# Kernel tuning notes

Hardware: AMD Instinct MI355X
Metric: run time of the kernel (lower is better)

## Reference

```python
import jax, jax.numpy as jnp
import numpy as np

FP8_MAX = 448.0  # finfo(float8_e4m3fn).max

def setup_inputs() -> dict:
    key = jax.random.key(0)
    k_x, k_w, k_b = jax.random.split(key, 3)
    B, S, D_IN, D_OUT = 4, 2048, 4096, 16384
    x = jax.random.normal(k_x, (B, S, D_IN), dtype=jnp.float32)
    # Build an fp8-quantized weight exactly as FP8WeightOnlyLinear.from_linear does:
    w = jax.random.normal(k_w, (D_OUT, D_IN), dtype=jnp.float32) * 0.02
    amax = jnp.max(jnp.abs(w))
    scale = jnp.where(amax > 0, amax / FP8_MAX, 1.0)
    # round-trip through float8_e4m3fn so stored values are true fp8 codes
    w_fp8 = jnp.clip(w / scale, -FP8_MAX, FP8_MAX).astype(jnp.float8_e4m3fn)
    weight_fp8 = w_fp8.astype(jnp.float32)  # fp8-representable values, held in fp32
    weight_scale = scale.reshape(1).astype(jnp.float32)
    bias = jax.random.normal(k_b, (D_OUT,), dtype=jnp.float32) * 0.01
    return {"x": x, "weight_fp8": weight_fp8, "weight_scale": weight_scale, "bias": bias}

def reference(x, weight_fp8, weight_scale, bias):
    # w = weight_fp8.to(x.dtype) * weight_scale ; out = x @ w.T + bias
    w = weight_fp8.astype(x.dtype) * weight_scale.astype(x.dtype)  # [D_OUT, D_IN]
    out = jnp.einsum('bsd,od->bso', x, w) + bias.astype(x.dtype)
    return out
```

## Files before the change

### kernel.cpp

```cpp
#include <hip/hip_runtime.h>
#include <stdint.h>

typedef unsigned int u32;
using i32x4 = __attribute__((ext_vector_type(4))) int;

#define GLD_LDS16(SRC, DST)                                      \
  __builtin_amdgcn_global_load_lds(                              \
      (const __attribute__((address_space(1))) void*)(SRC),      \
      (__attribute__((address_space(3))) void*)(DST), 16, 0, 0)

#define SCHED0() __builtin_amdgcn_sched_barrier(0)
#define BAR()    __builtin_amdgcn_s_barrier()
#define PRIO(x)  __builtin_amdgcn_s_setprio(x)

__global__ __launch_bounds__(256)
void quant_rows(const float* __restrict__ x, const float* __restrict__ w,
                signed char* __restrict__ xq, signed char* __restrict__ wq,
                float* __restrict__ sx, float* __restrict__ sw,
                int Mrows, int totRows, int K) {
  __shared__ float red[4];
  for (int row = blockIdx.x; row < totRows; row += gridDim.x) {
    const bool isx = row < Mrows;
    const float* src = isx ? x + (size_t)row * K : w + (size_t)(row - Mrows) * K;
    const float4* s4 = reinterpret_cast<const float4*>(src) + threadIdx.x * 4;
    float4 v[4];
#pragma unroll
    for (int g = 0; g < 4; ++g) v[g] = s4[g];
    float am = 0.f;
#pragma unroll
    for (int g = 0; g < 4; ++g)
      am = fmaxf(am, fmaxf(fmaxf(fabsf(v[g].x), fabsf(v[g].y)),
                           fmaxf(fabsf(v[g].z), fabsf(v[g].w))));
#pragma unroll
    for (int m = 1; m <= 32; m <<= 1) am = fmaxf(am, __shfl_xor(am, m));
    if ((threadIdx.x & 63) == 0) red[threadIdx.x >> 6] = am;
    __syncthreads();
    am = fmaxf(fmaxf(red[0], red[1]), fmaxf(red[2], red[3]));
    const float s   = am > 0.f ? am * (1.f / 127.f) : 1.f;
    const float inv = am > 0.f ? 127.f / am : 0.f;
    u32 pk[4];
#pragma unroll
    for (int g = 0; g < 4; ++g) {
      const float* vp = reinterpret_cast<const float*>(&v[g]);
      u32 p = 0;
#pragma unroll
      for (int e = 0; e < 4; ++e) {
        int q = (int)rintf(vp[e] * inv);
        q = q < -127 ? -127 : (q > 127 ? 127 : q);
        p |= ((u32)(q & 0xff)) << (8 * e);
      }
      pk[g] = p;
    }
    signed char* dst = (isx ? xq + (size_t)row * K : wq + (size_t)(row - Mrows) * K)
                       + threadIdx.x * 16;
    *reinterpret_cast<uint4*>(dst) = make_uint4(pk[0], pk[1], pk[2], pk[3]);
    if (threadIdx.x == 0) { if (isx) sx[row] = s; else sw[row - Mrows] = s; }
    __syncthreads();
  }
}

__global__ __launch_bounds__(512, 2)
void gemm_i8_gate(const signed char* __restrict__ A,
                  const signed char* __restrict__ B,
                  const float* __restrict__ sx,
                  const float* __restrict__ sw,
                  const float* __restrict__ wscale_p,
                  const float* __restrict__ bias,
                  float* __restrict__ C,
                  int Nn, int Kk, int NT) {
  __shared__ signed char lds[2][2][256 * 128];

  const int tid  = threadIdx.x;
  const int lane = tid & 63;
  const int wave = tid >> 6;
  const int wr = wave >> 2;
  const int wc = wave & 3;

  const int bid = blockIdx.x;
  const int cpx = gridDim.x >> 3;
  const int wg  = (bid & 7) * cpx + (bid >> 3);
  const int mt = wg / NT, nt = wg % NT;
  const int m0 = mt * 256, n0 = nt * 256;

  const int srow = lane >> 3;
  const int ss   = (lane & 7) ^ (srow & 7);
  const int r16  = lane & 15;
  const int kq   = lane >> 4;

  const signed char* ga = A + ((size_t)m0 + wave * 32 + srow) * Kk + ss * 16;
  const signed char* gb = B + ((size_t)n0 + wave * 32 + srow) * Kk + ss * 16;

  const int aoff = (wr * 128 + r16) * 128 + ((kq ^ (r16 & 7)) << 4);
  const int boff = (wc * 64  + r16) * 128 + ((kq ^ (r16 & 7)) << 4);

  i32x4 acc[8][4];
#pragma unroll
  for (int i = 0; i < 8; ++i)
#pragma unroll
    for (int j = 0; j < 4; ++j)
      acc[i][j] = (i32x4){0, 0, 0, 0};

  i32x4 afA[4], afB[4];
  i32x4 bP[4], bQ[4];

#define STAGE128(bfi_, op_, kt_) do {                                           \
    const signed char* _g = ((op_) ? gb : ga) + (size_t)(kt_) * 128;            \
    signed char* _d = &lds[bfi_][op_][wave * 32 * 128];                         \
    GLD_LDS16(_g,                    _d);                                       \
    GLD_LDS16(_g + (size_t)8  * Kk,  _d + 1024);                                \
    GLD_LDS16(_g + (size_t)16 * Kk,  _d + 2048);                                \
    GLD_LDS16(_g + (size_t)24 * Kk,  _d + 3072);                                \
  } while (0)

#define LDFA(AF_, la_, mh_, ks_) do {                                           \
    _Pragma("unroll") for (int _i = 0; _i < 4; ++_i)                            \
      AF_[_i] = *reinterpret_cast<const i32x4*>(                                \
          (la_) + ((aoff + ((mh_) * 4 + _i) * 2048) ^ ((ks_) << 6)));           \
  } while (0)

#define LDFB(BF_, lb_, ks_) do {                                                \
    _Pragma("unroll") for (int _n = 0; _n < 4; ++_n)                            \
      BF_[_n] = *reinterpret_cast<const i32x4*>(                                \
          (lb_) + ((boff + _n * 2048) ^ ((ks_) << 6)));                         \
  } while (0)

#define MFMAC(mh_, AF_, BF_)                                                    \
  _Pragma("unroll") for (int i = 0; i < 4; ++i)                                 \
  _Pragma("unroll") for (int n = 0; n < 4; ++n)                                 \
    acc[(mh_) * 4 + i][n] = __builtin_amdgcn_mfma_i32_16x16x64_i8(              \
        AF_[i], BF_[n], acc[(mh_) * 4 + i][n], 0, 0, 0)

  const int KT = Kk >> 7;

  STAGE128(0, 0, 0); STAGE128(0, 1, 0);
  STAGE128(1, 1, 1);
  STAGE128(1, 0, 1);
  asm volatile("s_waitcnt vmcnt(8)" ::: "memory");
  SCHED0(); BAR(); SCHED0();
  LDFA(afA, (const signed char*)&lds[0][0][0], 0, 0);
  LDFB(bP,  (const signed char*)&lds[0][1][0], 0);
  LDFB(bQ,  (const signed char*)&lds[0][1][0], 1);

#define TILE128(t_, CUR_) do {                                                  \
    const signed char* laC = &lds[CUR_][0][0];                                  \
    const signed char* laN = &lds[(CUR_) ^ 1][0][0];                            \
    const signed char* lbN = &lds[(CUR_) ^ 1][1][0];                            \
    const int kt2 = ((t_) + 2 < KT) ? (t_) + 2 : KT - 1;                        \
                                                        \
    SCHED0(); BAR(); SCHED0();                                                  \
    STAGE128(CUR_, 1, kt2);                       \
    LDFA(afB, laC, 1, 0);                                                       \
    PRIO(1); MFMAC(0, afA, bP); PRIO(0);                       \
    LDFA(afA, laC, 0, 1);                                                       \
    PRIO(1); MFMAC(1, afB, bP); PRIO(0);                       \
    LDFA(afB, laC, 1, 1);                                                       \
    SCHED0();                                                                   \
    asm volatile("s_waitcnt vmcnt(8)" ::: "memory");         \
                                                        \
    SCHED0(); BAR(); SCHED0();                                                  \
    STAGE128(CUR_, 0, kt2);                       \
    LDFB(bP, lbN, 0);                          \
    PRIO(1); MFMAC(0, afA, bQ); PRIO(0);                       \
    SCHED0();                                                                   \
    asm volatile("s_waitcnt vmcnt(8)" ::: "memory");         \
    SCHED0();                                                                   \
    LDFA(afA, laN, 0, 0);                          \
    PRIO(1); MFMAC(1, afB, bQ); PRIO(0);                       \
    LDFB(bQ, lbN, 1);                                \
  } while (0)

  for (int t = 0; t < KT; t += 2) {
    TILE128(t,     0);
    TILE128(t + 1, 1);
  }

  const float wsc = wscale_p[0];
  float cw[4], bv[4];
#pragma unroll
  for (int ni = 0; ni < 4; ++ni) {
    const int col = n0 + wc * 64 + ni * 16 + r16;
    cw[ni] = sw[col] * wsc;
    bv[ni] = bias[col];
  }
#pragma unroll
  for (int mi = 0; mi < 8; ++mi) {
#pragma unroll
    for (int r = 0; r < 4; ++r) {
      const int row = m0 + wr * 128 + mi * 16 + kq * 4 + r;
      const float sxr = sx[row];
      float* cp = C + (size_t)row * Nn + (n0 + wc * 64 + r16);
#pragma unroll
      for (int ni = 0; ni < 4; ++ni)
        cp[ni * 16] = (float)acc[mi][ni][r] * (sxr * cw[ni]) + bv[ni];
    }
  }
#undef STAGE128
#undef LDFA
#undef LDFB
#undef MFMAC
#undef TILE128
}

extern "C" void kernel_launch(void* const* d_in, const int* in_sizes, int n_in,
                              void* d_out, int out_size, void* d_ws, size_t ws_size,
                              hipStream_t stream) {
  (void)n_in; (void)out_size; (void)ws_size;
  const float* x  = (const float*)d_in[0];
  const float* w  = (const float*)d_in[1];
  const float* sc = (const float*)d_in[2];
  const float* bs = (const float*)d_in[3];
  float* out = (float*)d_out;

  const int N = in_sizes[3];
  const int K = in_sizes[1] / N;
  const int M = in_sizes[0] / K;

  signed char* xq = (signed char*)d_ws;
  signed char* wq = xq + (size_t)M * K;
  float* sxp = (float*)(wq + (size_t)N * K);
  float* swp = sxp + M;

  quant_rows<<<M + N, 256, 0, stream>>>(x, w, xq, wq, sxp, swp, M, M + N, K);

  const int NT = N / 256;
  const int nwg = (M / 256) * NT;
  gemm_i8_gate<<<nwg, 512, 0, stream>>>(xq, wq, sxp, swp, sc, bs, out, N, K, NT);
}
```

Measured before the change: 633.4 us.

## Switch int8 GEMM to 4-wave blocks with 128x128 per-wave tiles

Cuts the GEMM workgroup from 8 waves to 4, so each wave computes a 128x128 output tile (8x8 MFMA accumulators) instead of 128x64. The aim is to reuse each LDS fragment load across more MFMAs and cut LDS read traffic per output. The main loop is reordered so A and B fragments alternate in a 2x2 half pattern, and both operands are staged together later in the tile. The cost is much higher register pressure per wave with one block per CU, which lowers occupancy and leaves fewer waves to hide latency.

```diff
diff --git a/kernel.cpp b/kernel.cpp
--- a/kernel.cpp
+++ b/kernel.cpp
@@ -59,22 +59,22 @@
   }
 }
 
-__global__ __launch_bounds__(512, 2)
-void gemm_i8_gate(const signed char* __restrict__ A,
-                  const signed char* __restrict__ B,
-                  const float* __restrict__ sx,
-                  const float* __restrict__ sw,
-                  const float* __restrict__ wscale_p,
-                  const float* __restrict__ bias,
-                  float* __restrict__ C,
-                  int Nn, int Kk, int NT) {
+__global__ __launch_bounds__(256, 1)
+void gemm_i8_sq(const signed char* __restrict__ A,
+                const signed char* __restrict__ B,
+                const float* __restrict__ sx,
+                const float* __restrict__ sw,
+                const float* __restrict__ wscale_p,
+                const float* __restrict__ bias,
+                float* __restrict__ C,
+                int Nn, int Kk, int NT) {
   __shared__ signed char lds[2][2][256 * 128];
 
   const int tid  = threadIdx.x;
   const int lane = tid & 63;
   const int wave = tid >> 6;
-  const int wr = wave >> 2;
-  const int wc = wave & 3;
+  const int wr = wave >> 1;
+  const int wc = wave & 1;
 
   const int bid = blockIdx.x;
   const int cpx = gridDim.x >> 3;
@@ -87,98 +87,101 @@
   const int r16  = lane & 15;
   const int kq   = lane >> 4;
 
-  const signed char* ga = A + ((size_t)m0 + wave * 32 + srow) * Kk + ss * 16;
-  const signed char* gb = B + ((size_t)n0 + wave * 32 + srow) * Kk + ss * 16;
+  const signed char* ga = A + ((size_t)m0 + wave * 64 + srow) * Kk + ss * 16;
+  const signed char* gb = B + ((size_t)n0 + wave * 64 + srow) * Kk + ss * 16;
 
   const int aoff = (wr * 128 + r16) * 128 + ((kq ^ (r16 & 7)) << 4);
-  const int boff = (wc * 64  + r16) * 128 + ((kq ^ (r16 & 7)) << 4);
-
-  i32x4 acc[8][4];
+  const int boff = (wc * 128 + r16) * 128 + ((kq ^ (r16 & 7)) << 4);
+
+  i32x4 acc[8][8];
 #pragma unroll
   for (int i = 0; i < 8; ++i)
 #pragma unroll
-    for (int j = 0; j < 4; ++j)
+    for (int j = 0; j < 8; ++j)
       acc[i][j] = (i32x4){0, 0, 0, 0};
 
-  i32x4 afA[4], afB[4];
-  i32x4 bP[4], bQ[4];
-
-#define STAGE128(bfi_, op_, kt_) do {                                           \
+  i32x4 aF[4], aG[4];
+  i32x4 bF[4], bG[4];
+
+#define STAGE8(bfi_, op_, kt_) do {                                             \
     const signed char* _g = ((op_) ? gb : ga) + (size_t)(kt_) * 128;            \
-    signed char* _d = &lds[bfi_][op_][wave * 32 * 128];                         \
-    GLD_LDS16(_g,                    _d);                                       \
-    GLD_LDS16(_g + (size_t)8  * Kk,  _d + 1024);                                \
-    GLD_LDS16(_g + (size_t)16 * Kk,  _d + 2048);                                \
-    GLD_LDS16(_g + (size_t)24 * Kk,  _d + 3072);                                \
-  } while (0)
-
-#define LDFA(AF_, la_, mh_, ks_) do {                                           \
+    signed char* _d = &lds[bfi_][op_][wave * 64 * 128];                         \
+    _Pragma("unroll") for (int _j = 0; _j < 8; ++_j)                            \
+      GLD_LDS16(_g + (size_t)(_j * 8) * Kk, _d + _j * 1024);                    \
+  } while (0)
+
+#define LDF_A(AF_, la_, mh_, ks_) do {                                          \
     _Pragma("unroll") for (int _i = 0; _i < 4; ++_i)                            \
       AF_[_i] = *reinterpret_cast<const i32x4*>(                                \
           (la_) + ((aoff + ((mh_) * 4 + _i) * 2048) ^ ((ks_) << 6)));           \
   } while (0)
 
-#define LDFB(BF_, lb_, ks_) do {                                                \
+#define LDF_B(BF_, lb_, nh_, ks_) do {                                          \
     _Pragma("unroll") for (int _n = 0; _n < 4; ++_n)                            \
       BF_[_n] = *reinterpret_cast<const i32x4*>(                                \
-          (lb_) + ((boff + _n * 2048) ^ ((ks_) << 6)));                         \
-  } while (0)
-
-#define MFMAC(mh_, AF_, BF_)                                                    \
+          (lb_) + ((boff + ((nh_) * 4 + _n) * 2048) ^ ((ks_) << 6)));           \
+  } while (0)
+
+#define MFMAC(mh_, nh_, AF_, BF_)                                               \
   _Pragma("unroll") for (int i = 0; i < 4; ++i)                                 \
   _Pragma("unroll") for (int n = 0; n < 4; ++n)                                 \
-    acc[(mh_) * 4 + i][n] = __builtin_amdgcn_mfma_i32_16x16x64_i8(              \
-        AF_[i], BF_[n], acc[(mh_) * 4 + i][n], 0, 0, 0)
+    acc[(mh_) * 4 + i][(nh_) * 4 + n] = __builtin_amdgcn_mfma_i32_16x16x64_i8(  \
+        AF_[i], BF_[n], acc[(mh_) * 4 + i][(nh_) * 4 + n], 0, 0, 0)
 
   const int KT = Kk >> 7;
 
-  STAGE128(0, 0, 0); STAGE128(0, 1, 0);
-  STAGE128(1, 1, 1);
-  STAGE128(1, 0, 1);
-  asm volatile("s_waitcnt vmcnt(8)" ::: "memory");
+  STAGE8(0, 0, 0); STAGE8(0, 1, 0);
+  STAGE8(1, 0, 1); STAGE8(1, 1, 1);
+  asm volatile("s_waitcnt vmcnt(16)" ::: "memory");
   SCHED0(); BAR(); SCHED0();
-  LDFA(afA, (const signed char*)&lds[0][0][0], 0, 0);
-  LDFB(bP,  (const signed char*)&lds[0][1][0], 0);
-  LDFB(bQ,  (const signed char*)&lds[0][1][0], 1);
-
-#define TILE128(t_, CUR_) do {                                                  \
+  LDF_A(aF, (const signed char*)&lds[0][0][0], 0, 0);
+  LDF_B(bF, (const signed char*)&lds[0][1][0], 0, 0);
+
+#define TILE(t_, CUR_) do {                                                     \
     const signed char* laC = &lds[CUR_][0][0];                                  \
+    const signed char* lbC = &lds[CUR_][1][0];                                  \
     const signed char* laN = &lds[(CUR_) ^ 1][0][0];                            \
     const signed char* lbN = &lds[(CUR_) ^ 1][1][0];                            \
     const int kt2 = ((t_) + 2 < KT) ? (t_) + 2 : KT - 1;                        \
-                                                        \
+                             \
     SCHED0(); BAR(); SCHED0();                                                  \
-    STAGE128(CUR_, 1, kt2);                       \
-    LDFA(afB, laC, 1, 0);                                                       \
-    PRIO(1); MFMAC(0, afA, bP); PRIO(0);                       \
-    LDFA(afA, laC, 0, 1);                                                       \
-    PRIO(1); MFMAC(1, afB, bP); PRIO(0);                       \
-    LDFA(afB, laC, 1, 1);                                                       \
+    PRIO(1); MFMAC(0, 0, aF, bF); PRIO(0);                 \
+    LDF_B(bG, lbC, 1, 0);                                                       \
+    PRIO(1); MFMAC(0, 1, aF, bG); PRIO(0);                 \
+    LDF_A(aG, laC, 1, 0);                                                       \
+    PRIO(1); MFMAC(1, 0, aG, bF); PRIO(0);                 \
+    LDF_A(aF, laC, 0, 1);                                                       \
+    PRIO(1); MFMAC(1, 1, aG, bG); PRIO(0);                 \
+    LDF_B(bF, lbC, 0, 1);                                                       \
+    PRIO(1); MFMAC(0, 0, aF, bF); PRIO(0);                 \
+    LDF_B(bG, lbC, 1, 1);                                                       \
+    PRIO(1); MFMAC(0, 1, aF, bG); PRIO(0);                 \
+    LDF_A(aG, laC, 1, 1);                                                       \
     SCHED0();                                                                   \
     asm volatile("s_waitcnt vmcnt(8)" ::: "memory");         \
-                                                        \
+                    \
     SCHED0(); BAR(); SCHED0();                                                  \
-    STAGE128(CUR_, 0, kt2);                       \
-    LDFB(bP, lbN, 0);                          \
-    PRIO(1); MFMAC(0, afA, bQ); PRIO(0);                       \
+    STAGE8(CUR_, 0, kt2);                                      \
+    STAGE8(CUR_, 1, kt2);                                      \
+    LDF_A(aF, laN, 0, 0);                                     \
+    PRIO(1); MFMAC(1, 0, aG, bF); PRIO(0);                 \
     SCHED0();                                                                   \
-    asm volatile("s_waitcnt vmcnt(8)" ::: "memory");         \
+    asm volatile("s_waitcnt vmcnt(16)" ::: "memory");        \
     SCHED0();                                                                   \
-    LDFA(afA, laN, 0, 0);                          \
-    PRIO(1); MFMAC(1, afB, bQ); PRIO(0);                       \
-    LDFB(bQ, lbN, 1);                                \
+    LDF_B(bF, lbN, 0, 0);                                     \
+    PRIO(1); MFMAC(1, 1, aG, bG); PRIO(0);                 \
   } while (0)
 
   for (int t = 0; t < KT; t += 2) {
-    TILE128(t,     0);
-    TILE128(t + 1, 1);
+    TILE(t,     0);
+    TILE(t + 1, 1);
   }
 
   const float wsc = wscale_p[0];
-  float cw[4], bv[4];
-#pragma unroll
-  for (int ni = 0; ni < 4; ++ni) {
-    const int col = n0 + wc * 64 + ni * 16 + r16;
+  float cw[8], bv[8];
+#pragma unroll
+  for (int ni = 0; ni < 8; ++ni) {
+    const int col = n0 + wc * 128 + ni * 16 + r16;
     cw[ni] = sw[col] * wsc;
     bv[ni] = bias[col];
   }
@@ -188,17 +191,17 @@
     for (int r = 0; r < 4; ++r) {
       const int row = m0 + wr * 128 + mi * 16 + kq * 4 + r;
       const float sxr = sx[row];
-      float* cp = C + (size_t)row * Nn + (n0 + wc * 64 + r16);
-#pragma unroll
-      for (int ni = 0; ni < 4; ++ni)
+      float* cp = C + (size_t)row * Nn + (n0 + wc * 128 + r16);
+#pragma unroll
+      for (int ni = 0; ni < 8; ++ni)
         cp[ni * 16] = (float)acc[mi][ni][r] * (sxr * cw[ni]) + bv[ni];
     }
   }
-#undef STAGE128
-#undef LDFA
-#undef LDFB
+#undef STAGE8
+#undef LDF_A
+#undef LDF_B
 #undef MFMAC
-#undef TILE128
+#undef TILE
 }
 
 extern "C" void kernel_launch(void* const* d_in, const int* in_sizes, int n_in,
@@ -224,5 +227,5 @@
 
   const int NT = N / 256;
   const int nwg = (M / 256) * NT;
-  gemm_i8_gate<<<nwg, 512, 0, stream>>>(xq, wq, sxp, swp, sc, bs, out, N, K, NT);
+  gemm_i8_sq<<<nwg, 256, 0, stream>>>(xq, wq, sxp, swp, sc, bs, out, N, K, NT);
 }
```

After: 731.1 us. 15.4% more time.
